# Performance work log

Hardware: AMD Instinct MI355X
Metric: run time of the kernel (lower is better)

## Reference

```python
import jax, jax.numpy as jnp
import numpy as np

N, E, DM, H, DFF = 20000, 640000, 512, 8, 2048
DK = DM // H


def _layernorm(x, g, b, eps=1e-5):
    mu = jnp.mean(x, axis=-1, keepdims=True)
    var = jnp.mean(jnp.square(x - mu), axis=-1, keepdims=True)
    return (x - mu) * jax.lax.rsqrt(var + eps) * g + b


def setup_inputs() -> dict:
    key = jax.random.key(0)
    ks = jax.random.split(key, 12)
    s = 0.02
    h = jax.random.normal(ks[0], (N, DM), dtype=jnp.float32)
    src = jax.random.randint(ks[1], (E,), 0, N, dtype=jnp.int32)
    dst = jnp.sort(jax.random.randint(ks[2], (E,), 0, N, dtype=jnp.int32))
    return {
        "h": h,
        "src": src,
        "dst": dst,
        "Wq": jax.random.normal(ks[3], (DM, DM), dtype=jnp.float32) * s,
        "Wk": jax.random.normal(ks[4], (DM, DM), dtype=jnp.float32) * s,
        "Wv": jax.random.normal(ks[5], (DM, DM), dtype=jnp.float32) * s,
        "Wo": jax.random.normal(ks[6], (DM, DM), dtype=jnp.float32) * s,
        "ln1_g": jnp.ones((DM,), jnp.float32),
        "ln1_b": jnp.zeros((DM,), jnp.float32),
        "ln2_g": jnp.ones((DM,), jnp.float32),
        "ln2_b": jnp.zeros((DM,), jnp.float32),
        "W1": jax.random.normal(ks[7], (DM, DFF), dtype=jnp.float32) * s,
        "b1": jnp.zeros((DFF,), jnp.float32),
        "W2": jax.random.normal(ks[8], (DFF, DM), dtype=jnp.float32) * s,
        "b2": jnp.zeros((DM,), jnp.float32),
    }


def reference(h, src, dst, Wq, Wk, Wv, Wo, ln1_g, ln1_b, ln2_g, ln2_b, W1, b1, W2, b2):
    n = h.shape[0]
    # q/k/v projections (MaskedMMCSR equivalent score: k[src] . q[dst])
    q = (h @ Wq).reshape(n, H, DK)
    k = (h @ Wk).reshape(n, H, DK)
    v = (h @ Wv).reshape(n, H, DK)
    e = jnp.einsum("ehd,ehd->eh", k[src], q[dst]) / np.sqrt(DK).astype(np.float32)  # [E,H]
    # SparseSoftmax: softmax over incoming edges of each dst node
    m = jax.ops.segment_max(e, dst, num_segments=n)  # [n,H]
    ex = jnp.exp(e - m[dst])
    z = jax.ops.segment_sum(ex, dst, num_segments=n)
    attn = ex / z[dst]  # [E,H]
    # VectorSPMM: a[dst] = sum_e attn[e] * v[src[e]]
    a = jax.ops.segment_sum(attn[:, :, None] * v[src], dst, num_segments=n)
    a = a.reshape(n, DM)
    o = a @ Wo
    x = _layernorm(h + o, ln1_g, ln1_b)
    f = jax.nn.relu(x @ W1 + b1) @ W2 + b2
    return _layernorm(x + f, ln2_g, ln2_b)
```

## Files before the change

### kernel.cpp

```cpp
#include <hip/hip_runtime.h>
#include <cstdint>
#include <cstddef>

#define DMODEL 512
#define NHEAD 8
#define DFFN 2048
#define CHUNK 256

typedef float  floatx4  __attribute__((ext_vector_type(4)));
typedef short  shortx8  __attribute__((ext_vector_type(8)));
typedef unsigned short ushortx4 __attribute__((ext_vector_type(4)));
typedef unsigned short ushortx8 __attribute__((ext_vector_type(8)));

__device__ __forceinline__ float bf2f(unsigned short u) {
  union { unsigned int i; float f; } v; v.i = ((unsigned int)u) << 16; return v.f;
}
__device__ __forceinline__ unsigned short f2bf(float x) {
  union { float f; unsigned int i; } v; v.f = x;
  unsigned int r = v.i + 0x7fffu + ((v.i >> 16) & 1u);
  return (unsigned short)(r >> 16);
}

__device__ __forceinline__ void gload_lds16(const unsigned short* g, unsigned short* l) {
  __builtin_amdgcn_global_load_lds(
      (const __attribute__((address_space(1))) void*)g,
      (__attribute__((address_space(3))) void*)l,
      16, 0, 0);
}


__global__ void k_cast_bf16(const float* __restrict__ in, unsigned short* __restrict__ out, int n4)
{
  const int i = blockIdx.x * blockDim.x + threadIdx.x;
  if (i >= n4) return;
  const floatx4 v = *(const floatx4*)(in + (size_t)i * 4);
  ushortx4 o;
#pragma unroll
  for (int j = 0; j < 4; ++j) o[j] = f2bf(v[j]);
  *(ushortx4*)(out + (size_t)i * 4) = o;
}

__global__ void k_transpose_cast(const float* __restrict__ W, unsigned short* __restrict__ out, int K, int Nn)
{
  const int idx = blockIdx.x * blockDim.x + threadIdx.x;
  if (idx >= K * Nn) return;
  const int k = idx / Nn, n = idx - k * Nn;
  out[(size_t)n * K + k] = f2bf(W[idx]);
}

__global__ void k_row_ptr(const int* __restrict__ dst, int* __restrict__ rowp, int N_, int E_)
{
  const int i = blockIdx.x * blockDim.x + threadIdx.x;
  if (i > N_) return;
  int lo = 0, hi = E_;
  while (lo < hi) { const int mid = (lo + hi) >> 1; if (dst[mid] < i) lo = mid + 1; else hi = mid; }
  rowp[i] = lo;
}


template <typename OutT, bool HAS_BIAS, bool RELU>
__global__ __launch_bounds__(256) void k_gemm(
    const unsigned short* __restrict__ A,
    const unsigned short* __restrict__ BT,
    OutT* __restrict__ C,
    const float* __restrict__ bias,
    int M, int Nn, int K)
{
  __shared__ __align__(16) unsigned short As[128 * 32];
  __shared__ __align__(16) unsigned short Bs[128 * 32];
  const int tid  = threadIdx.x;
  const int wid  = tid >> 6;
  const int lane = tid & 63;
  const int wm = wid >> 1, wn = wid & 1;
  const int m0 = blockIdx.x * 128, n0 = blockIdx.y * 128;

  floatx4 acc[4][4];
#pragma unroll
  for (int i = 0; i < 4; ++i)
#pragma unroll
    for (int j = 0; j < 4; ++j) acc[i][j] = (floatx4)(0.0f);

  const int srow = lane >> 2;
  const int scol = (lane & 3) * 8;
  const int fr   = lane & 15;
  const int fk   = (lane >> 4) * 8;

  for (int k0 = 0; k0 < K; k0 += 32) {
#pragma unroll
    for (int jj = 0; jj < 2; ++jj) {
      const int c = jj * 4 + wid;
      int ra = m0 + c * 16 + srow;
      if (ra > M - 1) ra = M - 1;
      gload_lds16(A + (size_t)ra * K + k0 + scol, &As[c * 512 + lane * 8]);
      const int rb = n0 + c * 16 + srow;
      gload_lds16(BT + (size_t)rb * K + k0 + scol, &Bs[c * 512 + lane * 8]);
    }
    __syncthreads();

    shortx8 af[4], bfr[4];
#pragma unroll
    for (int i = 0; i < 4; ++i)
      af[i] = *(const shortx8*)&As[(wm * 64 + i * 16 + fr) * 32 + fk];
#pragma unroll
    for (int j = 0; j < 4; ++j)
      bfr[j] = *(const shortx8*)&Bs[(wn * 64 + j * 16 + fr) * 32 + fk];
#pragma unroll
    for (int i = 0; i < 4; ++i)
#pragma unroll
      for (int j = 0; j < 4; ++j)
        acc[i][j] = __builtin_amdgcn_mfma_f32_16x16x32_bf16(af[i], bfr[j], acc[i][j], 0, 0, 0);
    __syncthreads();
  }

  const int cr = (lane >> 4) * 4;
  const int cc = lane & 15;
#pragma unroll
  for (int j = 0; j < 4; ++j) {
    const int col = n0 + wn * 64 + j * 16 + cc;
    float bv = 0.0f;
    if (HAS_BIAS) bv = bias[col];
#pragma unroll
    for (int i = 0; i < 4; ++i) {
      const int rb = m0 + wm * 64 + i * 16 + cr;
#pragma unroll
      for (int r = 0; r < 4; ++r) {
        const int row = rb + r;
        if (row < M) {
          float v = acc[i][j][r];
          if (HAS_BIAS) v += bv;
          if (RELU) v = fmaxf(v, 0.0f);
          if constexpr (sizeof(OutT) == 2) C[(size_t)row * Nn + col] = f2bf(v);
          else                             C[(size_t)row * Nn + col] = v;
        }
      }
    }
  }
}


__global__ __launch_bounds__(256) void k_attn_fused(
    const unsigned short* __restrict__ qkv,
    const int* __restrict__ src, const int* __restrict__ rowp,
    unsigned short* __restrict__ a_bf, int N_)
{
  const int n = blockIdx.x;
  const int tid = threadIdx.x;
  const int wv = tid >> 6, lane = tid & 63;
  const int r0 = rowp[n], r1 = rowp[n + 1];
  const int deg = r1 - r0;

  __shared__ __align__(16) unsigned short q_lds[DMODEL];
  __shared__ int   s_src[CHUNK];
  __shared__ float s_raw[CHUNK * NHEAD];
  __shared__ float s_m[NHEAD], s_mnew[NHEAD], s_scale[NHEAD];

  if (tid < 64)
    *(ushortx8*)&q_lds[tid * 8] = *(const ushortx8*)(qkv + (size_t)n * 1536 + tid * 8);
  if (tid < NHEAD) s_m[tid] = -3.0e38f;
  __syncthreads();

  float qr[8];
  {
    const ushortx8 qf = *(const ushortx8*)&q_lds[lane * 8];
#pragma unroll
    for (int i = 0; i < 8; ++i) qr[i] = bf2f(qf[i]);
  }

  const int head = lane >> 3, sub = lane & 7;
  const int hh = tid >> 5;
  const int d0 = tid * 2;

  float a0 = 0.0f, a1 = 0.0f, z = 0.0f;

  for (int c0 = 0; c0 < deg; c0 += CHUNK) {
    const int clen = min(CHUNK, deg - c0);

    if (tid < clen) s_src[tid] = src[r0 + c0 + tid];
    __syncthreads();

    for (int i = wv; i < clen; i += 4) {
      const int s = s_src[i];
      const ushortx8 kf = *(const ushortx8*)(qkv + (size_t)s * 1536 + 512 + lane * 8);
      float acc = 0.0f;
#pragma unroll
      for (int t = 0; t < 8; ++t) acc += qr[t] * bf2f(kf[t]);
      acc += __shfl_xor(acc, 1);
      acc += __shfl_xor(acc, 2);
      acc += __shfl_xor(acc, 4);
      if (sub == 0) s_raw[i * 8 + head] = acc * 0.125f;
    }
    __syncthreads();

    if (wv == 0) {
      const int h = lane & 7;
      float mx = -3.0e38f;
      for (int j = lane >> 3; j < clen; j += 8) mx = fmaxf(mx, s_raw[j * 8 + h]);
      mx = fmaxf(mx, __shfl_xor(mx, 8));
      mx = fmaxf(mx, __shfl_xor(mx, 16));
      mx = fmaxf(mx, __shfl_xor(mx, 32));
      if (lane < NHEAD) {
        const float mo = s_m[h];
        const float mn = fmaxf(mo, mx);
        s_mnew[h] = mn;
        s_scale[h] = __expf(mo - mn);
        s_m[h] = mn;
      }
    }
    __syncthreads();

    {
      const float sc = s_scale[hh];
      a0 *= sc; a1 *= sc; z *= sc;
      const int tot = clen * 8;
      for (int idx = tid; idx < tot; idx += 256) {
        const int h = idx & 7;
        s_raw[idx] = __expf(s_raw[idx] - s_mnew[h]);
      }
    }
    __syncthreads();

    const unsigned short* vbase = qkv + 1024 + d0;
    int j = 0;
    for (; j + 4 <= clen; j += 4) {
      const unsigned int v0 = *(const unsigned int*)(vbase + (size_t)s_src[j]     * 1536);
      const unsigned int v1 = *(const unsigned int*)(vbase + (size_t)s_src[j + 1] * 1536);
      const unsigned int v2 = *(const unsigned int*)(vbase + (size_t)s_src[j + 2] * 1536);
      const unsigned int v3 = *(const unsigned int*)(vbase + (size_t)s_src[j + 3] * 1536);
      const float p0 = s_raw[(j)     * 8 + hh];
      const float p1 = s_raw[(j + 1) * 8 + hh];
      const float p2 = s_raw[(j + 2) * 8 + hh];
      const float p3 = s_raw[(j + 3) * 8 + hh];
      a0 += p0 * bf2f((unsigned short)(v0 & 0xffffu));
      a1 += p0 * bf2f((unsigned short)(v0 >> 16));
      a0 += p1 * bf2f((unsigned short)(v1 & 0xffffu));
      a1 += p1 * bf2f((unsigned short)(v1 >> 16));
      a0 += p2 * bf2f((unsigned short)(v2 & 0xffffu));
      a1 += p2 * bf2f((unsigned short)(v2 >> 16));
      a0 += p3 * bf2f((unsigned short)(v3 & 0xffffu));
      a1 += p3 * bf2f((unsigned short)(v3 >> 16));
      z += p0 + p1 + p2 + p3;
    }
    for (; j < clen; ++j) {
      const unsigned int vv = *(const unsigned int*)(vbase + (size_t)s_src[j] * 1536);
      const float p = s_raw[j * 8 + hh];
      a0 += p * bf2f((unsigned short)(vv & 0xffffu));
      a1 += p * bf2f((unsigned short)(vv >> 16));
      z += p;
    }
    __syncthreads();
  }

  const float invz = (z > 0.0f) ? 1.0f / z : 0.0f;
  const unsigned int lo = f2bf(a0 * invz);
  const unsigned int hi = f2bf(a1 * invz);
  *(unsigned int*)(a_bf + (size_t)n * 512 + d0) = lo | (hi << 16);
}


template <bool WRITE_BF>
__global__ __launch_bounds__(256) void k_ln(
    const float* __restrict__ xa, const float* __restrict__ xb,
    const float* __restrict__ g, const float* __restrict__ b,
    float* __restrict__ out_f, unsigned short* __restrict__ out_bf, int n_rows)
{
  const int row = blockIdx.x * 4 + (threadIdx.x >> 6);
  if (row >= n_rows) return;
  const int lane = threadIdx.x & 63;
  const float* pa = xa + (size_t)row * DMODEL + lane * 8;
  const float* pb = xb + (size_t)row * DMODEL + lane * 8;
  float v[8];
  {
    floatx4 a0 = *(const floatx4*)pa;
    floatx4 a1 = *(const floatx4*)(pa + 4);
    floatx4 b0 = *(const floatx4*)pb;
    floatx4 b1 = *(const floatx4*)(pb + 4);
#pragma unroll
    for (int j = 0; j < 4; ++j) { v[j] = a0[j] + b0[j]; v[4 + j] = a1[j] + b1[j]; }
  }
  float s = 0.0f;
#pragma unroll
  for (int j = 0; j < 8; ++j) s += v[j];
#pragma unroll
  for (int d = 1; d < 64; d <<= 1) s += __shfl_xor(s, d);
  const float mu = s * (1.0f / DMODEL);
  float q = 0.0f;
#pragma unroll
  for (int j = 0; j < 8; ++j) { const float t = v[j] - mu; q += t * t; }
#pragma unroll
  for (int d = 1; d < 64; d <<= 1) q += __shfl_xor(q, d);
  const float rs = rsqrtf(q * (1.0f / DMODEL) + 1e-5f);
  const float* gp = g + lane * 8;
  const float* bp = b + lane * 8;
  floatx4 g0 = *(const floatx4*)gp, g1 = *(const floatx4*)(gp + 4);
  floatx4 h0 = *(const floatx4*)bp, h1 = *(const floatx4*)(bp + 4);
  float o[8];
#pragma unroll
  for (int j = 0; j < 4; ++j) {
    o[j]     = (v[j]     - mu) * rs * g0[j] + h0[j];
    o[4 + j] = (v[4 + j] - mu) * rs * g1[j] + h1[j];
  }
  float* po = out_f + (size_t)row * DMODEL + lane * 8;
  *(floatx4*)po       = (floatx4){o[0], o[1], o[2], o[3]};
  *(floatx4*)(po + 4) = (floatx4){o[4], o[5], o[6], o[7]};
  if (WRITE_BF) {
    ushortx8 ob;
#pragma unroll
    for (int j = 0; j < 8; ++j) ob[j] = f2bf(o[j]);
    *(ushortx8*)(out_bf + (size_t)row * DMODEL + lane * 8) = ob;
  }
}


extern "C" void kernel_launch(void* const* d_in, const int* in_sizes, int n_in,
                              void* d_out, int out_size, void* d_ws, size_t ws_size,
                              hipStream_t stream)
{
  (void)n_in; (void)out_size; (void)ws_size;
  const float* h    = (const float*)d_in[0];
  const int*   src  = (const int*)  d_in[1];
  const int*   dst  = (const int*)  d_in[2];
  const float* Wq   = (const float*)d_in[3];
  const float* Wk   = (const float*)d_in[4];
  const float* Wv   = (const float*)d_in[5];
  const float* Wo   = (const float*)d_in[6];
  const float* ln1g = (const float*)d_in[7];
  const float* ln1b = (const float*)d_in[8];
  const float* ln2g = (const float*)d_in[9];
  const float* ln2b = (const float*)d_in[10];
  const float* W1   = (const float*)d_in[11];
  const float* b1   = (const float*)d_in[12];
  const float* W2   = (const float*)d_in[13];
  const float* b2   = (const float*)d_in[14];

  const int N_ = in_sizes[0] / DMODEL;
  const int E_ = in_sizes[1];

  char* ws = (char*)d_ws;
  size_t off = 0;
  auto alloc = [&](size_t bytes) -> void* {
    void* p = ws + off;
    off += (bytes + 255) & ~(size_t)255;
    return p;
  };

  char* regA = (char*)alloc((size_t)N_ * DMODEL * 2);
  char* regB = (char*)alloc((size_t)N_ * DFFN * 2);
  char* regC = (char*)alloc((size_t)N_ * DMODEL * 4);
  char* regD = (char*)alloc((size_t)N_ * DMODEL * 2);
  char* regE = (char*)alloc((size_t)N_ * DMODEL * 4);

  unsigned short* qkvT  = (unsigned short*)alloc((size_t)1536 * 512 * 2);
  unsigned short* WoT   = (unsigned short*)alloc((size_t)512 * 512 * 2);
  unsigned short* W1T   = (unsigned short*)alloc((size_t)2048 * 512 * 2);
  unsigned short* W2T   = (unsigned short*)alloc((size_t)512 * 2048 * 2);
  int*            rowp  = (int*)alloc((size_t)(N_ + 1) * 4);

  unsigned short* h_bf  = (unsigned short*)regA;
  unsigned short* qkv   = (unsigned short*)regB;
  unsigned short* midbf = (unsigned short*)regB;
  float*          o     = (float*)regC;
  float*          f     = (float*)regC;
  unsigned short* a_bf  = (unsigned short*)regD;
  unsigned short* x_bf  = (unsigned short*)regD;
  float*          x     = (float*)regE;

  {
    const int n4 = N_ * DMODEL / 4;
    k_cast_bf16<<<(n4 + 255) / 256, 256, 0, stream>>>(h, h_bf, n4);
  }
  k_transpose_cast<<<(512 * 512 + 255) / 256, 256, 0, stream>>>(Wq, qkvT + 0 * 512 * 512, 512, 512);
  k_transpose_cast<<<(512 * 512 + 255) / 256, 256, 0, stream>>>(Wk, qkvT + 1 * 512 * 512, 512, 512);
  k_transpose_cast<<<(512 * 512 + 255) / 256, 256, 0, stream>>>(Wv, qkvT + 2 * 512 * 512, 512, 512);
  k_transpose_cast<<<(512 * 512 + 255) / 256, 256, 0, stream>>>(Wo, WoT, 512, 512);
  k_transpose_cast<<<(512 * 2048 + 255) / 256, 256, 0, stream>>>(W1, W1T, 512, 2048);
  k_transpose_cast<<<(512 * 2048 + 255) / 256, 256, 0, stream>>>(W2, W2T, 2048, 512);
  k_row_ptr<<<(N_ + 1 + 255) / 256, 256, 0, stream>>>(dst, rowp, N_, E_);

  const int mt = (N_ + 127) / 128;
  k_gemm<unsigned short, false, false><<<dim3(mt, 1536 / 128), 256, 0, stream>>>(h_bf, qkvT, qkv, nullptr, N_, 1536, 512);
  k_attn_fused<<<N_, 256, 0, stream>>>(qkv, src, rowp, a_bf, N_);
  k_gemm<float, false, false><<<dim3(mt, 512 / 128), 256, 0, stream>>>(a_bf, WoT, o, nullptr, N_, 512, 512);
  k_ln<true><<<(N_ + 3) / 4, 256, 0, stream>>>(h, o, ln1g, ln1b, x, x_bf, N_);
  k_gemm<unsigned short, true, true><<<dim3(mt, 2048 / 128), 256, 0, stream>>>(x_bf, W1T, midbf, b1, N_, 2048, 512);
  k_gemm<float, true, false><<<dim3(mt, 512 / 128), 256, 0, stream>>>(midbf, W2T, f, b2, N_, 512, 2048);
  k_ln<false><<<(N_ + 3) / 4, 256, 0, stream>>>(x, f, ln2g, ln2b, (float*)d_out, nullptr, N_);
}
```

Measured before the change: 637.6 us.

## Swizzle 64-wide GEMM K tiles and drop online max from edge softmax

The GEMM now stages 64-wide K tiles per barrier instead of 32, using an XOR-swizzled LDS layout so that fragment reads avoid bank conflicts. This halves the number of __syncthreads per K and gives two MFMA sub-steps per tile. The attention kernel drops the per-chunk running max, rescale and separate exp pass. It exponentiates scores directly in the score loop and processes two edges per wave iteration for more memory-level parallelism. Skipping the max subtraction risks exp overflow if scores grow large, so correctness depends on the scores staying bounded.

After: 615.2 us. -3.5%, faster.

```diff
diff --git a/kernel.cpp b/kernel.cpp
--- a/kernel.cpp
+++ b/kernel.cpp
@@ -66,8 +66,8 @@
     const float* __restrict__ bias,
     int M, int Nn, int K)
 {
-  __shared__ __align__(16) unsigned short As[128 * 32];
-  __shared__ __align__(16) unsigned short Bs[128 * 32];
+  __shared__ __align__(16) unsigned short As[128 * 64];
+  __shared__ __align__(16) unsigned short Bs[128 * 64];
   const int tid  = threadIdx.x;
   const int wid  = tid >> 6;
   const int lane = tid & 63;
@@ -80,35 +80,45 @@
 #pragma unroll
     for (int j = 0; j < 4; ++j) acc[i][j] = (floatx4)(0.0f);
 
-  const int srow = lane >> 2;
-  const int scol = (lane & 3) * 8;
-  const int fr   = lane & 15;
-  const int fk   = (lane >> 4) * 8;
-
-  for (int k0 = 0; k0 < K; k0 += 32) {
-#pragma unroll
-    for (int jj = 0; jj < 2; ++jj) {
-      const int c = jj * 4 + wid;
-      int ra = m0 + c * 16 + srow;
+  const int srow  = tid >> 3;
+  const int scolb = ((tid & 7) ^ (srow & 7)) * 8;
+  const int fr = lane & 15;
+  const int fb = lane >> 4;
+  const int fx = fr & 7;
+
+  const int arow[4] = { (wm * 64 +  0 + fr) * 64, (wm * 64 + 16 + fr) * 64,
+                        (wm * 64 + 32 + fr) * 64, (wm * 64 + 48 + fr) * 64 };
+  const int brow[4] = { (wn * 64 +  0 + fr) * 64, (wn * 64 + 16 + fr) * 64,
+                        (wn * 64 + 32 + fr) * 64, (wn * 64 + 48 + fr) * 64 };
+
+  for (int k0 = 0; k0 < K; k0 += 64) {
+#pragma unroll
+    for (int r = 0; r < 4; ++r) {
+      int ra = m0 + r * 32 + srow;
       if (ra > M - 1) ra = M - 1;
-      gload_lds16(A + (size_t)ra * K + k0 + scol, &As[c * 512 + lane * 8]);
-      const int rb = n0 + c * 16 + srow;
-      gload_lds16(BT + (size_t)rb * K + k0 + scol, &Bs[c * 512 + lane * 8]);
-    }
-    __syncthreads();
-
-    shortx8 af[4], bfr[4];
-#pragma unroll
-    for (int i = 0; i < 4; ++i)
-      af[i] = *(const shortx8*)&As[(wm * 64 + i * 16 + fr) * 32 + fk];
-#pragma unroll
-    for (int j = 0; j < 4; ++j)
-      bfr[j] = *(const shortx8*)&Bs[(wn * 64 + j * 16 + fr) * 32 + fk];
-#pragma unroll
-    for (int i = 0; i < 4; ++i)
-#pragma unroll
-      for (int j = 0; j < 4; ++j)
-        acc[i][j] = __builtin_amdgcn_mfma_f32_16x16x32_bf16(af[i], bfr[j], acc[i][j], 0, 0, 0);
+      gload_lds16(A + (size_t)ra * K + k0 + scolb, &As[r * 2048 + tid * 8]);
+    }
+#pragma unroll
+    for (int r = 0; r < 4; ++r) {
+      const int rb = n0 + r * 32 + srow;
+      gload_lds16(BT + (size_t)rb * K + k0 + scolb, &Bs[r * 2048 + tid * 8]);
+    }
+    __syncthreads();
+
+#pragma unroll
+    for (int kk = 0; kk < 2; ++kk) {
+      const int blk = ((kk * 4 + fb) ^ fx) * 8;
+      shortx8 af[4], bfr[4];
+#pragma unroll
+      for (int i = 0; i < 4; ++i) af[i]  = *(const shortx8*)&As[arow[i] + blk];
+#pragma unroll
+      for (int j = 0; j < 4; ++j) bfr[j] = *(const shortx8*)&Bs[brow[j] + blk];
+#pragma unroll
+      for (int i = 0; i < 4; ++i)
+#pragma unroll
+        for (int j = 0; j < 4; ++j)
+          acc[i][j] = __builtin_amdgcn_mfma_f32_16x16x32_bf16(af[i], bfr[j], acc[i][j], 0, 0, 0);
+    }
     __syncthreads();
   }
 
@@ -149,19 +159,12 @@
   const int r0 = rowp[n], r1 = rowp[n + 1];
   const int deg = r1 - r0;
 
-  __shared__ __align__(16) unsigned short q_lds[DMODEL];
   __shared__ int   s_src[CHUNK];
   __shared__ float s_raw[CHUNK * NHEAD];
-  __shared__ float s_m[NHEAD], s_mnew[NHEAD], s_scale[NHEAD];
-
-  if (tid < 64)
-    *(ushortx8*)&q_lds[tid * 8] = *(const ushortx8*)(qkv + (size_t)n * 1536 + tid * 8);
-  if (tid < NHEAD) s_m[tid] = -3.0e38f;
-  __syncthreads();
 
   float qr[8];
   {
-    const ushortx8 qf = *(const ushortx8*)&q_lds[lane * 8];
+    const ushortx8 qf = *(const ushortx8*)(qkv + (size_t)n * 1536 + lane * 8);
 #pragma unroll
     for (int i = 0; i < 8; ++i) qr[i] = bf2f(qf[i]);
   }
@@ -178,43 +181,22 @@
     if (tid < clen) s_src[tid] = src[r0 + c0 + tid];
     __syncthreads();
 
-    for (int i = wv; i < clen; i += 4) {
-      const int s = s_src[i];
-      const ushortx8 kf = *(const ushortx8*)(qkv + (size_t)s * 1536 + 512 + lane * 8);
-      float acc = 0.0f;
-#pragma unroll
-      for (int t = 0; t < 8; ++t) acc += qr[t] * bf2f(kf[t]);
-      acc += __shfl_xor(acc, 1);
-      acc += __shfl_xor(acc, 2);
-      acc += __shfl_xor(acc, 4);
-      if (sub == 0) s_raw[i * 8 + head] = acc * 0.125f;
-    }
-    __syncthreads();
-
-    if (wv == 0) {
-      const int h = lane & 7;
-      float mx = -3.0e38f;
-      for (int j = lane >> 3; j < clen; j += 8) mx = fmaxf(mx, s_raw[j * 8 + h]);
-      mx = fmaxf(mx, __shfl_xor(mx, 8));
-      mx = fmaxf(mx, __shfl_xor(mx, 16));
-      mx = fmaxf(mx, __shfl_xor(mx, 32));
-      if (lane < NHEAD) {
-        const float mo = s_m[h];
-        const float mn = fmaxf(mo, mx);
-        s_mnew[h] = mn;
-        s_scale[h] = __expf(mo - mn);
-        s_m[h] = mn;
-      }
-    }
-    __syncthreads();
-
-    {
-      const float sc = s_scale[hh];
-      a0 *= sc; a1 *= sc; z *= sc;
-      const int tot = clen * 8;
-      for (int idx = tid; idx < tot; idx += 256) {
-        const int h = idx & 7;
-        s_raw[idx] = __expf(s_raw[idx] - s_mnew[h]);
+    for (int i = wv; i < clen; i += 8) {
+      const int i1 = (i + 4 < clen) ? i + 4 : i;
+      const int s0 = s_src[i], s1 = s_src[i1];
+      const ushortx8 kf0 = *(const ushortx8*)(qkv + (size_t)s0 * 1536 + 512 + lane * 8);
+      const ushortx8 kf1 = *(const ushortx8*)(qkv + (size_t)s1 * 1536 + 512 + lane * 8);
+      float acc0 = 0.0f, acc1 = 0.0f;
+#pragma unroll
+      for (int t = 0; t < 8; ++t) acc0 += qr[t] * bf2f(kf0[t]);
+#pragma unroll
+      for (int t = 0; t < 8; ++t) acc1 += qr[t] * bf2f(kf1[t]);
+      acc0 += __shfl_xor(acc0, 1); acc1 += __shfl_xor(acc1, 1);
+      acc0 += __shfl_xor(acc0, 2); acc1 += __shfl_xor(acc1, 2);
+      acc0 += __shfl_xor(acc0, 4); acc1 += __shfl_xor(acc1, 4);
+      if (sub == 0) {
+        s_raw[i * 8 + head] = __expf(acc0 * 0.125f);
+        if (i1 != i) s_raw[i1 * 8 + head] = __expf(acc1 * 0.125f);
       }
     }
     __syncthreads();
```
